# Kernel tuning notes

Hardware: AMD Instinct MI355X
Metric: run time of the kernel (lower is better)

The kernel has to match this reference:

```python
import jax, jax.numpy as jnp
import numpy as np

D_K = 64


def setup_inputs() -> dict:
    key = jax.random.key(0)
    kq, kk, kv, km = jax.random.split(key, 4)
    B, H, S = 4, 16, 2048
    Q = jax.random.normal(kq, (B, H, S, D_K), dtype=jnp.float32)
    K = jax.random.normal(kk, (B, H, S, D_K), dtype=jnp.float32)
    V = jax.random.normal(kv, (B, H, S, D_K), dtype=jnp.float32)
    # boolean mask, True = masked out; broadcast over heads
    mask = jax.random.randint(km, (B, 1, S, S), 0, 2).astype(jnp.bool_)
    return {"Q": Q, "K": K, "V": V, "mask": mask}


def reference(Q, K, V, mask):
    scale = jnp.sqrt(jnp.asarray(D_K, dtype=Q.dtype))
    # [B,H,S,S] scores
    scores = jnp.einsum('bhqd,bhkd->bhqk', Q, K) / scale
    scores = jnp.where(mask, jnp.asarray(-1e9, dtype=scores.dtype), scores)
    attn = jax.nn.softmax(scores, axis=-1)
    return jnp.einsum('bhqk,bhkd->bhqd', attn, V)
```

## Files before the change

### kernel.cpp

```cpp
#include <hip/hip_runtime.h>
#include <hip/hip_bf16.h>


#define SEQ   2048
#define DK    64
#define NB_   4
#define NBH   64
#define KVB   64
#define QB    128
#define NT    (SEQ / KVB)

#define MASKH_WORDS ((size_t)NB_ * SEQ * 64)

typedef float    f32x16 __attribute__((ext_vector_type(16)));
typedef _Float16 f16x8  __attribute__((ext_vector_type(8)));

#define QSCALE 0.18033688011112042f
#define MBIAS  (-5.0f)
#define CH     264

#if __has_builtin(__builtin_amdgcn_exp2f)
#define EXP2F(x) __builtin_amdgcn_exp2f(x)
#else
#define EXP2F(x) exp2f(x)
#endif

__device__ __forceinline__ unsigned pkrtz(float lo, float hi) {
  auto v = __builtin_amdgcn_cvt_pkrtz(lo, hi);
  return __builtin_bit_cast(unsigned, v);
}

#define BARRIER()                                          \
  do {                                                     \
    asm volatile("s_waitcnt lgkmcnt(0)" ::: "memory");     \
    __builtin_amdgcn_s_barrier();                          \
  } while (0)

__device__ __forceinline__ void halfswap(unsigned a, unsigned b,
                                         unsigned& out_lo, unsigned& out_hi, int hiL) {
#if __has_builtin(__builtin_amdgcn_permlane32_swap)
  auto r = __builtin_amdgcn_permlane32_swap(a, b, false, false);
  out_lo = r[0];
  out_hi = r[1];
#else
  unsigned ax = __shfl_xor(a, 32), bx = __shfl_xor(b, 32);
  out_lo = hiL ? bx : a;
  out_hi = hiL ? b : ax;
#endif
}

__global__ __launch_bounds__(256) void mask_pack2(const int* __restrict__ M,
                                                  unsigned* __restrict__ P) {
  int t  = blockIdx.x * 256 + threadIdx.x;
  int hi = t & 1, T = (t >> 1) & 31, q = (t >> 6) & 2047, b = t >> 17;
  const int* src = M + ((size_t)b * SEQ + q) * SEQ + T * 64 + 4 * hi;
  unsigned bits = 0;
#pragma unroll
  for (int kvb = 0; kvb < 2; ++kvb)
#pragma unroll
    for (int m = 0; m < 4; ++m) {
      int4 v = *(const int4*)(src + 32 * kvb + 8 * m);
      int sh = 16 * kvb + 4 * m;
      bits |= ((unsigned)(v.x != 0) << sh) | ((unsigned)(v.y != 0) << (sh + 1)) |
              ((unsigned)(v.z != 0) << (sh + 2)) | ((unsigned)(v.w != 0) << (sh + 3));
    }
  P[t] = bits;
}

template <bool PACKED>
__global__ __launch_bounds__(256) void sda_attn_kernel(
    const float* __restrict__ Q, const float* __restrict__ K,
    const float* __restrict__ V, const int* __restrict__ M,
    const unsigned* __restrict__ Mh, float* __restrict__ O) {
  __shared__ __align__(16) _Float16 Kl[2][16 * CH];
  __shared__ __align__(16) _Float16 Vt[2][16 * CH];

  const int bh   = blockIdx.x;
  const int qt   = blockIdx.y;
  const int b    = bh >> 4;
  const int tid  = threadIdx.x;
  const int wid  = tid >> 6;
  const int lane = tid & 63;
  const int lq   = lane & 31;
  const int hiL  = lane >> 5;

  const size_t base = (size_t)bh * SEQ * DK;
  const int    q    = qt * QB + wid * 32 + lq;

  f16x8 qf[4];
  {
    const float* qp = Q + base + (size_t)q * DK + hiL * 8;
#pragma unroll
    for (int kk = 0; kk < 4; ++kk) {
      float4 A  = *(const float4*)(qp + kk * 16);
      float4 Bv = *(const float4*)(qp + kk * 16 + 4);
      uint4 u;
      u.x = pkrtz(A.x * QSCALE, A.y * QSCALE);
      u.y = pkrtz(A.z * QSCALE, A.w * QSCALE);
      u.z = pkrtz(Bv.x * QSCALE, Bv.y * QSCALE);
      u.w = pkrtz(Bv.z * QSCALE, Bv.w * QSCALE);
      qf[kk] = __builtin_bit_cast(f16x8, u);
    }
  }

  f32x16 oacc[2];
#pragma unroll
  for (int db = 0; db < 2; ++db)
#pragma unroll
    for (int r = 0; r < 16; ++r) oacc[db][r] = 0.f;
  float lreg = 0.f;

  const int krow = tid >> 2, c0 = tid & 3;
  const int kp   = tid & 31, d8 = (tid >> 5) * 8;
  const float* Kg  = K + base + (size_t)krow * DK + c0 * 16;
  const float* Vg0 = V + base + (size_t)(2 * kp) * DK + d8;
  const float* Vg1 = Vg0 + DK;

  const int kwa = ((krow >> 5) * 8 + c0 * 2) * CH + (krow & 31) * 8;
  const int kwb = kwa + CH;
  const int vwb = ((d8 >> 5) * 8 + (kp >> 3) * 2 + ((kp >> 2) & 1)) * CH +
                  (d8 & 31) * 8 + (kp & 3) * 2;

  float4 kpre[4], vpre[4];
#define LOADT(kb_)                                                        \
  {                                                                       \
    const float* kg = Kg + (size_t)(kb_)*DK;                              \
    _Pragma("unroll") for (int i = 0; i < 4; ++i)                         \
        kpre[i] = *(const float4*)(kg + 4 * i);                           \
    const float* va = Vg0 + (size_t)(kb_)*DK;                             \
    const float* vb = Vg1 + (size_t)(kb_)*DK;                             \
    vpre[0] = *(const float4*)va; vpre[1] = *(const float4*)(va + 4);     \
    vpre[2] = *(const float4*)vb; vpre[3] = *(const float4*)(vb + 4);     \
  }

#define STAGE(b_)                                                         \
  {                                                                       \
    uint4 u0, u1;                                                         \
    u0.x = pkrtz(kpre[0].x, kpre[0].y); u0.y = pkrtz(kpre[0].z, kpre[0].w); \
    u0.z = pkrtz(kpre[1].x, kpre[1].y); u0.w = pkrtz(kpre[1].z, kpre[1].w); \
    u1.x = pkrtz(kpre[2].x, kpre[2].y); u1.y = pkrtz(kpre[2].z, kpre[2].w); \
    u1.z = pkrtz(kpre[3].x, kpre[3].y); u1.w = pkrtz(kpre[3].z, kpre[3].w); \
    *(uint4*)&Kl[b_][kwa] = u0;                                           \
    *(uint4*)&Kl[b_][kwb] = u1;                                           \
    const float* va_ = (const float*)&vpre[0];                            \
    const float* vc_ = (const float*)&vpre[2];                            \
    _Pragma("unroll") for (int j = 0; j < 8; ++j)                         \
        *(unsigned*)&Vt[b_][vwb + j * 8] = pkrtz(va_[j], vc_[j]);         \
  }

  const unsigned* Mhp  = PACKED ? Mh + ((size_t)b * SEQ + q) * 64 + hiL : nullptr;
  const int*      Mrow = PACKED ? nullptr : M + ((size_t)b * SEQ + q) * SEQ + 4 * hiL;

  LOADT(0);
  STAGE(0);
  LOADT(KVB);
  unsigned mw_cur = PACKED ? Mhp[0] : 0u;
  BARRIER();

  for (int t = 0; t < NT; ++t) {
    const int cur = t & 1;

    f32x16 sc[2];
#pragma unroll
    for (int kvb = 0; kvb < 2; ++kvb)
#pragma unroll
      for (int r = 0; r < 16; ++r) sc[kvb][r] = MBIAS;

    __builtin_amdgcn_s_setprio(1);
#pragma unroll
    for (int kk = 0; kk < 4; ++kk)
#pragma unroll
      for (int kvb = 0; kvb < 2; ++kvb) {
        f16x8 kf = *(const f16x8*)&Kl[cur][(kvb * 8 + kk * 2 + hiL) * CH + lq * 8];
        sc[kvb] = __builtin_amdgcn_mfma_f32_32x32x16_f16(kf, qf[kk], sc[kvb], 0, 0, 0);
      }
    __builtin_amdgcn_s_setprio(0);

    const bool more = (t + 1 < NT);
    unsigned mw_next = 0;
    if (more) {
      STAGE(cur ^ 1);
      if (t + 2 < NT) LOADT((t + 2) * KVB);
      if (PACKED) mw_next = Mhp[2 * (t + 1)];
    }

    int4 mraw[8];
    if (!PACKED) {
#pragma unroll
      for (int kvb = 0; kvb < 2; ++kvb)
#pragma unroll
        for (int m = 0; m < 4; ++m)
          mraw[kvb * 4 + m] = *(const int4*)(Mrow + t * KVB + 32 * kvb + 8 * m);
    }

    float rs = 0.f;
    unsigned pr[2][4][2];
#pragma unroll
    for (int kvb = 0; kvb < 2; ++kvb) {
      float e[16];
#pragma unroll
      for (int r = 0; r < 16; ++r) {
        float ev = EXP2F(sc[kvb][r]);
        bool msk;
        if (PACKED) {
          msk = ((mw_cur >> (16 * kvb + r)) & 1u) != 0u;
        } else {
          int4 v = mraw[kvb * 4 + (r >> 2)];
          int mm = (r & 3) == 0 ? v.x : (r & 3) == 1 ? v.y : (r & 3) == 2 ? v.z : v.w;
          msk = mm != 0;
        }
        ev = msk ? 0.f : ev;
        e[r] = ev;
        rs += ev;
      }
#pragma unroll
      for (int m = 0; m < 4; ++m) {
        pr[kvb][m][0] = pkrtz(e[4 * m + 0], e[4 * m + 1]);
        pr[kvb][m][1] = pkrtz(e[4 * m + 2], e[4 * m + 3]);
      }
    }

    {
      unsigned ru = __builtin_bit_cast(unsigned, rs), plo, phi;
      halfswap(ru, ru, plo, phi, hiL);
      float other = __builtin_bit_cast(float, hiL ? plo : phi);
      lreg += rs + other;
    }

#pragma unroll
    for (int ks = 0; ks < 4; ++ks) {
      const int kvb = ks >> 1, ms = (ks & 1) * 2;
      unsigned w0, w1, w2, w3;
      halfswap(pr[kvb][ms][0], pr[kvb][ms + 1][0], w0, w2, hiL);
      halfswap(pr[kvb][ms][1], pr[kvb][ms + 1][1], w1, w3, hiL);
      f16x8 pf = __builtin_bit_cast(f16x8, make_uint4(w0, w1, w2, w3));

      __builtin_amdgcn_s_setprio(1);
#pragma unroll
      for (int db = 0; db < 2; ++db) {
        f16x8 vf = *(const f16x8*)&Vt[cur][(db * 8 + ks * 2 + hiL) * CH + lq * 8];
        oacc[db] = __builtin_amdgcn_mfma_f32_32x32x16_f16(vf, pf, oacc[db], 0, 0, 0);
      }
      __builtin_amdgcn_s_setprio(0);
    }

    mw_cur = mw_next;
    if (more) BARRIER();
  }

  float inv = (lreg > 0.f) ? 1.0f / lreg : 0.f;
  float* op = O + base + (size_t)q * DK + 4 * hiL;
#pragma unroll
  for (int db = 0; db < 2; ++db)
#pragma unroll
    for (int m = 0; m < 4; ++m) {
      float4 o;
      o.x = oacc[db][4 * m + 0] * inv;
      o.y = oacc[db][4 * m + 1] * inv;
      o.z = oacc[db][4 * m + 2] * inv;
      o.w = oacc[db][4 * m + 3] * inv;
      *(float4*)(op + 32 * db + 8 * m) = o;
    }
}

extern "C" void kernel_launch(void* const* d_in, const int* in_sizes, int n_in,
                              void* d_out, int out_size, void* d_ws, size_t ws_size,
                              hipStream_t stream) {
  const float* Q = (const float*)d_in[0];
  const float* K = (const float*)d_in[1];
  const float* V = (const float*)d_in[2];
  const int*   M = (const int*)d_in[3];
  float*       O = (float*)d_out;
  dim3 grid(NBH, SEQ / QB);

  if (ws_size >= MASKH_WORDS * 4) {
    unsigned* Mh = (unsigned*)d_ws;
    mask_pack2<<<(int)(MASKH_WORDS / 256), 256, 0, stream>>>(M, Mh);
    sda_attn_kernel<true><<<grid, 256, 0, stream>>>(Q, K, V, M, Mh, O);
  } else {
    sda_attn_kernel<false><<<grid, 256, 0, stream>>>(Q, K, V, M, nullptr, O);
  }
}
```

Baseline: 144.9 us.

## Pre-convert K/V to fp16 MFMA layout and stream via global_load_lds

Adds two pre-pass kernels that convert K and V to fp16 in the exact tile layout the MFMA loop reads, stored in workspace. The main attention kernel then copies tiles straight into LDS with global_load_lds, with no register staging or in-loop conversion, and waits on vmcnt before each barrier. The row sum now uses fdot2 on the packed fp16 probabilities, and the constant score bias is dropped (initial scores zero). This trades extra launches and a full K/V read+write pass for a lighter inner loop. The fallback path keeps the old structure.

```diff
diff --git a/kernel.cpp b/kernel.cpp
--- a/kernel.cpp
+++ b/kernel.cpp
@@ -11,24 +11,35 @@
 #define NT    (SEQ / KVB)
 
 #define MASKH_WORDS ((size_t)NB_ * SEQ * 64)
+#define WSK_OFF ((size_t)2 * 1024 * 1024)
+#define WSV_OFF ((size_t)18 * 1024 * 1024)
+#define WS_NEED ((size_t)34 * 1024 * 1024)
 
 typedef float    f32x16 __attribute__((ext_vector_type(16)));
 typedef _Float16 f16x8  __attribute__((ext_vector_type(8)));
+typedef _Float16 f16x2v __attribute__((ext_vector_type(2)));
 
 #define QSCALE 0.18033688011112042f
-#define MBIAS  (-5.0f)
-#define CH     264
 
 #if __has_builtin(__builtin_amdgcn_exp2f)
 #define EXP2F(x) __builtin_amdgcn_exp2f(x)
 #else
-#define EXP2F(x) exp2f(x)
+__device__ __forceinline__ float EXP2F(float x) {
+  float r;
+  asm("v_exp_f32 %0, %1\n\ts_nop 1" : "=v"(r) : "v"(x));
+  return r;
+}
 #endif
 
 __device__ __forceinline__ unsigned pkrtz(float lo, float hi) {
   auto v = __builtin_amdgcn_cvt_pkrtz(lo, hi);
   return __builtin_bit_cast(unsigned, v);
 }
+
+#define GLOAD16(g, l)                                                          \
+  __builtin_amdgcn_global_load_lds(                                            \
+      (const __attribute__((address_space(1))) unsigned*)(g),                  \
+      (__attribute__((address_space(3))) unsigned*)(l), 16, 0, 0)
 
 #define BARRIER()                                          \
   do {                                                     \
@@ -49,6 +60,7 @@
 #endif
 }
 
+
 __global__ __launch_bounds__(256) void mask_pack2(const int* __restrict__ M,
                                                   unsigned* __restrict__ P) {
   int t  = blockIdx.x * 256 + threadIdx.x;
@@ -67,13 +79,39 @@
   P[t] = bits;
 }
 
-template <bool PACKED>
-__global__ __launch_bounds__(256) void sda_attn_kernel(
-    const float* __restrict__ Q, const float* __restrict__ K,
-    const float* __restrict__ V, const int* __restrict__ M,
-    const unsigned* __restrict__ Mh, float* __restrict__ O) {
-  __shared__ __align__(16) _Float16 Kl[2][16 * CH];
-  __shared__ __align__(16) _Float16 Vt[2][16 * CH];
+__global__ __launch_bounds__(256) void k_relayout(const float* __restrict__ K,
+                                                  _Float16* __restrict__ W) {
+  int t  = blockIdx.x * 256 + threadIdx.x;
+  int lq = t & 31, c = (t >> 5) & 15, kt = (t >> 9) & 31, bh = t >> 14;
+  int kv = kt * 64 + (c >> 3) * 32 + lq;
+  int d0 = ((c >> 1) & 3) * 16 + (c & 1) * 8;
+  const float4* src = (const float4*)(K + ((size_t)bh * SEQ + kv) * DK + d0);
+  float4 a = src[0], b4 = src[1];
+  uint4 o = { pkrtz(a.x, a.y), pkrtz(a.z, a.w), pkrtz(b4.x, b4.y), pkrtz(b4.z, b4.w) };
+  *(uint4*)(W + (size_t)t * 8) = o;
+}
+
+__global__ __launch_bounds__(256) void v_relayout(const float* __restrict__ V,
+                                                  _Float16* __restrict__ W) {
+  int t  = blockIdx.x * 256 + threadIdx.x;
+  int lq = t & 31, c = (t >> 5) & 15, kt = (t >> 9) & 31, bh = t >> 14;
+  int kv0 = kt * 64 + ((c >> 1) & 3) * 16 + (c & 1) * 8;
+  int d   = (c >> 3) * 32 + lq;
+  const float* vp = V + ((size_t)bh * SEQ + kv0) * DK + d;
+  float v[8];
+#pragma unroll
+  for (int j = 0; j < 8; ++j) v[j] = vp[(size_t)j * DK];
+  uint4 o = { pkrtz(v[0], v[1]), pkrtz(v[2], v[3]), pkrtz(v[4], v[5]), pkrtz(v[6], v[7]) };
+  *(uint4*)(W + (size_t)t * 8) = o;
+}
+
+
+__global__ __launch_bounds__(256) void sda_attn_pc(
+    const float* __restrict__ Q, const unsigned* __restrict__ Mh,
+    const _Float16* __restrict__ wsK, const _Float16* __restrict__ wsV,
+    float* __restrict__ O) {
+  __shared__ __align__(16) _Float16 Kl[2][16 * 256];
+  __shared__ __align__(16) _Float16 Vt[2][16 * 256];
 
   const int bh   = blockIdx.x;
   const int qt   = blockIdx.y;
@@ -110,88 +148,54 @@
     for (int r = 0; r < 16; ++r) oacc[db][r] = 0.f;
   float lreg = 0.f;
 
-  const int krow = tid >> 2, c0 = tid & 3;
-  const int kp   = tid & 31, d8 = (tid >> 5) * 8;
-  const float* Kg  = K + base + (size_t)krow * DK + c0 * 16;
-  const float* Vg0 = V + base + (size_t)(2 * kp) * DK + d8;
-  const float* Vg1 = Vg0 + DK;
-
-  const int kwa = ((krow >> 5) * 8 + c0 * 2) * CH + (krow & 31) * 8;
-  const int kwb = kwa + CH;
-  const int vwb = ((d8 >> 5) * 8 + (kp >> 3) * 2 + ((kp >> 2) & 1)) * CH +
-                  (d8 & 31) * 8 + (kp & 3) * 2;
-
-  float4 kpre[4], vpre[4];
-#define LOADT(kb_)                                                        \
-  {                                                                       \
-    const float* kg = Kg + (size_t)(kb_)*DK;                              \
-    _Pragma("unroll") for (int i = 0; i < 4; ++i)                         \
-        kpre[i] = *(const float4*)(kg + 4 * i);                           \
-    const float* va = Vg0 + (size_t)(kb_)*DK;                             \
-    const float* vb = Vg1 + (size_t)(kb_)*DK;                             \
-    vpre[0] = *(const float4*)va; vpre[1] = *(const float4*)(va + 4);     \
-    vpre[2] = *(const float4*)vb; vpre[3] = *(const float4*)(vb + 4);     \
-  }
-
-#define STAGE(b_)                                                         \
-  {                                                                       \
-    uint4 u0, u1;                                                         \
-    u0.x = pkrtz(kpre[0].x, kpre[0].y); u0.y = pkrtz(kpre[0].z, kpre[0].w); \
-    u0.z = pkrtz(kpre[1].x, kpre[1].y); u0.w = pkrtz(kpre[1].z, kpre[1].w); \
-    u1.x = pkrtz(kpre[2].x, kpre[2].y); u1.y = pkrtz(kpre[2].z, kpre[2].w); \
-    u1.z = pkrtz(kpre[3].x, kpre[3].y); u1.w = pkrtz(kpre[3].z, kpre[3].w); \
-    *(uint4*)&Kl[b_][kwa] = u0;                                           \
-    *(uint4*)&Kl[b_][kwb] = u1;                                           \
-    const float* va_ = (const float*)&vpre[0];                            \
-    const float* vc_ = (const float*)&vpre[2];                            \
-    _Pragma("unroll") for (int j = 0; j < 8; ++j)                         \
-        *(unsigned*)&Vt[b_][vwb + j * 8] = pkrtz(va_[j], vc_[j]);         \
-  }
-
-  const unsigned* Mhp  = PACKED ? Mh + ((size_t)b * SEQ + q) * 64 + hiL : nullptr;
-  const int*      Mrow = PACKED ? nullptr : M + ((size_t)b * SEQ + q) * SEQ + 4 * hiL;
-
-  LOADT(0);
-  STAGE(0);
-  LOADT(KVB);
-  unsigned mw_cur = PACKED ? Mhp[0] : 0u;
+  const _Float16* skb = wsK + (size_t)bh * 32 * 4096 + wid * 1024 + lane * 8;
+  const _Float16* svb = wsV + (size_t)bh * 32 * 4096 + wid * 1024 + lane * 8;
+
+#define STAGE_GL(buf_, kt_)                                   \
+  {                                                           \
+    const _Float16* sk = skb + (size_t)(kt_) * 4096;          \
+    const _Float16* sv = svb + (size_t)(kt_) * 4096;          \
+    _Float16* dk = &Kl[buf_][wid * 1024];                     \
+    _Float16* dv = &Vt[buf_][wid * 1024];                     \
+    GLOAD16(sk, dk);                                          \
+    GLOAD16(sk + 512, dk + 512);                              \
+    GLOAD16(sv, dv);                                          \
+    GLOAD16(sv + 512, dv + 512);                              \
+  }
+
+  const unsigned* Mhp = Mh + ((size_t)b * SEQ + q) * 64 + hiL;
+  const f16x2v ones = {(_Float16)1.0f, (_Float16)1.0f};
+  (void)ones;
+
+  STAGE_GL(0, 0);
+  unsigned mw_cur = Mhp[0];
+  asm volatile("s_waitcnt vmcnt(0)" ::: "memory");
   BARRIER();
 
   for (int t = 0; t < NT; ++t) {
-    const int cur = t & 1;
-
-    f32x16 sc[2];
-#pragma unroll
-    for (int kvb = 0; kvb < 2; ++kvb)
-#pragma unroll
-      for (int r = 0; r < 16; ++r) sc[kvb][r] = MBIAS;
-
-    __builtin_amdgcn_s_setprio(1);
-#pragma unroll
-    for (int kk = 0; kk < 4; ++kk)
-#pragma unroll
-      for (int kvb = 0; kvb < 2; ++kvb) {
-        f16x8 kf = *(const f16x8*)&Kl[cur][(kvb * 8 + kk * 2 + hiL) * CH + lq * 8];
-        sc[kvb] = __builtin_amdgcn_mfma_f32_32x32x16_f16(kf, qf[kk], sc[kvb], 0, 0, 0);
-      }
-    __builtin_amdgcn_s_setprio(0);
-
+    const int  cur  = t & 1;
     const bool more = (t + 1 < NT);
     unsigned mw_next = 0;
     if (more) {
-      STAGE(cur ^ 1);
-      if (t + 2 < NT) LOADT((t + 2) * KVB);
-      if (PACKED) mw_next = Mhp[2 * (t + 1)];
-    }
-
-    int4 mraw[8];
-    if (!PACKED) {
-#pragma unroll
-      for (int kvb = 0; kvb < 2; ++kvb)
-#pragma unroll
-        for (int m = 0; m < 4; ++m)
-          mraw[kvb * 4 + m] = *(const int4*)(Mrow + t * KVB + 32 * kvb + 8 * m);
-    }
+      STAGE_GL(cur ^ 1, t + 1);
+      mw_next = Mhp[2 * (t + 1)];
+    }
+
+    f32x16 sc[2];
+#pragma unroll
+    for (int kvb = 0; kvb < 2; ++kvb)
+#pragma unroll
+      for (int r = 0; r < 16; ++r) sc[kvb][r] = 0.f;
+
+    __builtin_amdgcn_s_setprio(1);
+#pragma unroll
+    for (int kk = 0; kk < 4; ++kk)
+#pragma unroll
+      for (int kvb = 0; kvb < 2; ++kvb) {
+        f16x8 kf = *(const f16x8*)&Kl[cur][(kvb * 8 + kk * 2 + hiL) * 256 + lq * 8];
+        sc[kvb] = __builtin_amdgcn_mfma_f32_32x32x16_f16(kf, qf[kk], sc[kvb], 0, 0, 0);
+      }
+    __builtin_amdgcn_s_setprio(0);
 
     float rs = 0.f;
     unsigned pr[2][4][2];
@@ -201,22 +205,19 @@
 #pragma unroll
       for (int r = 0; r < 16; ++r) {
         float ev = EXP2F(sc[kvb][r]);
-        bool msk;
-        if (PACKED) {
-          msk = ((mw_cur >> (16 * kvb + r)) & 1u) != 0u;
-        } else {
-          int4 v = mraw[kvb * 4 + (r >> 2)];
-          int mm = (r & 3) == 0 ? v.x : (r & 3) == 1 ? v.y : (r & 3) == 2 ? v.z : v.w;
-          msk = mm != 0;
-        }
-        ev = msk ? 0.f : ev;
-        e[r] = ev;
-        rs += ev;
+        bool msk = ((mw_cur >> (16 * kvb + r)) & 1u) != 0u;
+        e[r] = msk ? 0.f : ev;
       }
 #pragma unroll
       for (int m = 0; m < 4; ++m) {
         pr[kvb][m][0] = pkrtz(e[4 * m + 0], e[4 * m + 1]);
         pr[kvb][m][1] = pkrtz(e[4 * m + 2], e[4 * m + 3]);
+#if __has_builtin(__builtin_amdgcn_fdot2)
+        rs = __builtin_amdgcn_fdot2(__builtin_bit_cast(f16x2v, pr[kvb][m][0]), ones, rs, false);
+        rs = __builtin_amdgcn_fdot2(__builtin_bit_cast(f16x2v, pr[kvb][m][1]), ones, rs, false);
+#else
+        rs += e[4 * m + 0] + e[4 * m + 1] + e[4 * m + 2] + e[4 * m + 3];
+#endif
       }
     }
 
@@ -238,16 +239,163 @@
       __builtin_amdgcn_s_setprio(1);
 #pragma unroll
       for (int db = 0; db < 2; ++db) {
+        f16x8 vf = *(const f16x8*)&Vt[cur][(db * 8 + ks * 2 + hiL) * 256 + lq * 8];
+        oacc[db] = __builtin_amdgcn_mfma_f32_32x32x16_f16(vf, pf, oacc[db], 0, 0, 0);
+      }
+      __builtin_amdgcn_s_setprio(0);
+    }
+
+    mw_cur = mw_next;
+    if (more) {
+      asm volatile("s_waitcnt vmcnt(0)" ::: "memory");
+      BARRIER();
+    }
+  }
+
+  float inv = (lreg > 0.f) ? 1.0f / lreg : 0.f;
+  float* op = O + base + (size_t)q * DK + 4 * hiL;
+#pragma unroll
+  for (int db = 0; db < 2; ++db)
+#pragma unroll
+    for (int m = 0; m < 4; ++m) {
+      float4 o;
+      o.x = oacc[db][4 * m + 0] * inv;
+      o.y = oacc[db][4 * m + 1] * inv;
+      o.z = oacc[db][4 * m + 2] * inv;
+      o.w = oacc[db][4 * m + 3] * inv;
+      *(float4*)(op + 32 * db + 8 * m) = o;
+    }
+}
+
+
+#define CH 264
+__global__ __launch_bounds__(256) void sda_attn_fb(
+    const float* __restrict__ Q, const float* __restrict__ K,
+    const float* __restrict__ V, const int* __restrict__ M,
+    float* __restrict__ O) {
+  __shared__ __align__(16) _Float16 Kl[2][16 * CH];
+  __shared__ __align__(16) _Float16 Vt[2][16 * CH];
+  const int bh = blockIdx.x, qt = blockIdx.y, b = bh >> 4;
+  const int tid = threadIdx.x, wid = tid >> 6, lane = tid & 63;
+  const int lq = lane & 31, hiL = lane >> 5;
+  const size_t base = (size_t)bh * SEQ * DK;
+  const int q = qt * QB + wid * 32 + lq;
+
+  f16x8 qf[4];
+  {
+    const float* qp = Q + base + (size_t)q * DK + hiL * 8;
+#pragma unroll
+    for (int kk = 0; kk < 4; ++kk) {
+      float4 A = *(const float4*)(qp + kk * 16), Bv = *(const float4*)(qp + kk * 16 + 4);
+      uint4 u = { pkrtz(A.x * QSCALE, A.y * QSCALE), pkrtz(A.z * QSCALE, A.w * QSCALE),
+                  pkrtz(Bv.x * QSCALE, Bv.y * QSCALE), pkrtz(Bv.z * QSCALE, Bv.w * QSCALE) };
+      qf[kk] = __builtin_bit_cast(f16x8, u);
+    }
+  }
+  f32x16 oacc[2];
+#pragma unroll
+  for (int db = 0; db < 2; ++db)
+#pragma unroll
+    for (int r = 0; r < 16; ++r) oacc[db][r] = 0.f;
+  float lreg = 0.f;
+
+  const int krow = tid >> 2, c0 = tid & 3, kp = tid & 31, d8 = (tid >> 5) * 8;
+  const float* Kg = K + base + (size_t)krow * DK + c0 * 16;
+  const float* Vg0 = V + base + (size_t)(2 * kp) * DK + d8;
+  const float* Vg1 = Vg0 + DK;
+  const int kwa = ((krow >> 5) * 8 + c0 * 2) * CH + (krow & 31) * 8;
+  const int kwb = kwa + CH;
+  const int vwb = ((d8 >> 5) * 8 + (kp >> 3) * 2 + ((kp >> 2) & 1)) * CH +
+                  (d8 & 31) * 8 + (kp & 3) * 2;
+  float4 kpre[4], vpre[4];
+#define FLOADT(kb_)                                                      \
+  {                                                                      \
+    const float* kg = Kg + (size_t)(kb_)*DK;                             \
+    _Pragma("unroll") for (int i = 0; i < 4; ++i)                        \
+        kpre[i] = *(const float4*)(kg + 4 * i);                          \
+    const float* va = Vg0 + (size_t)(kb_)*DK;                            \
+    const float* vb = Vg1 + (size_t)(kb_)*DK;                            \
+    vpre[0] = *(const float4*)va; vpre[1] = *(const float4*)(va + 4);    \
+    vpre[2] = *(const float4*)vb; vpre[3] = *(const float4*)(vb + 4);    \
+  }
+#define FSTAGE(b_)                                                          \
+  {                                                                         \
+    uint4 u0, u1;                                                           \
+    u0.x = pkrtz(kpre[0].x, kpre[0].y); u0.y = pkrtz(kpre[0].z, kpre[0].w); \
+    u0.z = pkrtz(kpre[1].x, kpre[1].y); u0.w = pkrtz(kpre[1].z, kpre[1].w); \
+    u1.x = pkrtz(kpre[2].x, kpre[2].y); u1.y = pkrtz(kpre[2].z, kpre[2].w); \
+    u1.z = pkrtz(kpre[3].x, kpre[3].y); u1.w = pkrtz(kpre[3].z, kpre[3].w); \
+    *(uint4*)&Kl[b_][kwa] = u0;                                             \
+    *(uint4*)&Kl[b_][kwb] = u1;                                             \
+    const float* va_ = (const float*)&vpre[0];                              \
+    const float* vc_ = (const float*)&vpre[2];                              \
+    _Pragma("unroll") for (int j = 0; j < 8; ++j)                           \
+        *(unsigned*)&Vt[b_][vwb + j * 8] = pkrtz(va_[j], vc_[j]);           \
+  }
+  const int* Mrow = M + ((size_t)b * SEQ + q) * SEQ + 4 * hiL;
+  FLOADT(0); FSTAGE(0); FLOADT(KVB);
+  BARRIER();
+  for (int t = 0; t < NT; ++t) {
+    const int cur = t & 1;
+    f32x16 sc[2];
+#pragma unroll
+    for (int kvb = 0; kvb < 2; ++kvb)
+#pragma unroll
+      for (int r = 0; r < 16; ++r) sc[kvb][r] = 0.f;
+#pragma unroll
+    for (int kk = 0; kk < 4; ++kk)
+#pragma unroll
+      for (int kvb = 0; kvb < 2; ++kvb) {
+        f16x8 kf = *(const f16x8*)&Kl[cur][(kvb * 8 + kk * 2 + hiL) * CH + lq * 8];
+        sc[kvb] = __builtin_amdgcn_mfma_f32_32x32x16_f16(kf, qf[kk], sc[kvb], 0, 0, 0);
+      }
+    const bool more = (t + 1 < NT);
+    if (more) { FSTAGE(cur ^ 1); if (t + 2 < NT) FLOADT((t + 2) * KVB); }
+    int4 mraw[8];
+#pragma unroll
+    for (int kvb = 0; kvb < 2; ++kvb)
+#pragma unroll
+      for (int m = 0; m < 4; ++m)
+        mraw[kvb * 4 + m] = *(const int4*)(Mrow + t * KVB + 32 * kvb + 8 * m);
+    float rs = 0.f;
+    unsigned pr[2][4][2];
+#pragma unroll
+    for (int kvb = 0; kvb < 2; ++kvb) {
+      float e[16];
+#pragma unroll
+      for (int r = 0; r < 16; ++r) {
+        float ev = EXP2F(sc[kvb][r]);
+        int4 v = mraw[kvb * 4 + (r >> 2)];
+        int mm = (r & 3) == 0 ? v.x : (r & 3) == 1 ? v.y : (r & 3) == 2 ? v.z : v.w;
+        ev = mm != 0 ? 0.f : ev;
+        e[r] = ev; rs += ev;
+      }
+#pragma unroll
+      for (int m = 0; m < 4; ++m) {
+        pr[kvb][m][0] = pkrtz(e[4 * m + 0], e[4 * m + 1]);
+        pr[kvb][m][1] = pkrtz(e[4 * m + 2], e[4 * m + 3]);
+      }
+    }
+    {
+      unsigned ru = __builtin_bit_cast(unsigned, rs), plo, phi;
+      halfswap(ru, ru, plo, phi, hiL);
+      lreg += rs + __builtin_bit_cast(float, hiL ? plo : phi);
+    }
+#pragma unroll
+    for (int ks = 0; ks < 4; ++ks) {
+      const int kvb = ks >> 1, ms = (ks & 1) * 2;
+      unsigned w0, w1, w2, w3;
+      halfswap(pr[kvb][ms][0], pr[kvb][ms + 1][0], w0, w2, hiL);
+      halfswap(pr[kvb][ms][1], pr[kvb][ms + 1][1], w1, w3, hiL);
+      f16x8 pf = __builtin_bit_cast(f16x8, make_uint4(w0, w1, w2, w3));
+#pragma unroll
+      for (int db = 0; db < 2; ++db) {
         f16x8 vf = *(const f16x8*)&Vt[cur][(db * 8 + ks * 2 + hiL) * CH + lq * 8];
         oacc[db] = __builtin_amdgcn_mfma_f32_32x32x16_f16(vf, pf, oacc[db], 0, 0, 0);
       }
-      __builtin_amdgcn_s_setprio(0);
-    }
-
-    mw_cur = mw_next;
+    }
     if (more) BARRIER();
   }
-
   float inv = (lreg > 0.f) ? 1.0f / lreg : 0.f;
   float* op = O + base + (size_t)q * DK + 4 * hiL;
 #pragma unroll
@@ -273,11 +421,15 @@
   float*       O = (float*)d_out;
   dim3 grid(NBH, SEQ / QB);
 
-  if (ws_size >= MASKH_WORDS * 4) {
-    unsigned* Mh = (unsigned*)d_ws;
+  if (ws_size >= WS_NEED) {
+    unsigned*  Mh  = (unsigned*)d_ws;
+    _Float16*  wsK = (_Float16*)((char*)d_ws + WSK_OFF);
+    _Float16*  wsV = (_Float16*)((char*)d_ws + WSV_OFF);
     mask_pack2<<<(int)(MASKH_WORDS / 256), 256, 0, stream>>>(M, Mh);
-    sda_attn_kernel<true><<<grid, 256, 0, stream>>>(Q, K, V, M, Mh, O);
+    k_relayout<<<4096, 256, 0, stream>>>(K, wsK);
+    v_relayout<<<4096, 256, 0, stream>>>(V, wsV);
+    sda_attn_pc<<<grid, 256, 0, stream>>>(Q, Mh, wsK, wsV, O);
   } else {
-    sda_attn_kernel<false><<<grid, 256, 0, stream>>>(Q, K, V, M, nullptr, O);
-  }
-}
+    sda_attn_fb<<<grid, 256, 0, stream>>>(Q, K, V, M, O);
+  }
+}
```

After: 152.2 us. +5.1%, slower.
